# Kernel optimization log

Hardware: AMD Instinct MI355X
Metric: run time of the kernel (lower is better)

## Reference

```python
import jax, jax.numpy as jnp
import numpy as np

B, T, D, N = 4, 2048, 1024, 8
H = D // N


def _rope_tables(t, d, dtype=jnp.float32):
    inv_freq = 1.0 / (10000.0 ** (jnp.arange(0, d, 2, dtype=jnp.float32) / d))
    pos = jnp.arange(t, dtype=jnp.float32)
    ang = jnp.einsum('i,j->ij', pos, inv_freq)  # [T, D/2]
    cos = jnp.concatenate([jnp.cos(ang), jnp.cos(ang)], axis=-1).astype(dtype)  # [T, D]
    sin = jnp.concatenate([jnp.sin(ang), jnp.sin(ang)], axis=-1).astype(dtype)
    return cos, sin


def setup_inputs() -> dict:
    key = jax.random.key(0)
    kx, kq, kk, kv = jax.random.split(key, 4)
    s = 1.0 / np.sqrt(D)
    x = jax.random.normal(kx, (B, T, D), dtype=jnp.float32)
    wq = jax.random.normal(kq, (D, D), dtype=jnp.float32) * s
    wk = jax.random.normal(kk, (D, D), dtype=jnp.float32) * s
    wv = jax.random.normal(kv, (D, D), dtype=jnp.float32) * s
    cos, sin = _rope_tables(T, D)
    return {"x": x, "wq": wq, "wk": wk, "wv": wv, "cos": cos, "sin": sin}


def _rotate_half(z):
    # torch: view(..., -1, 2); x1=even idx, x2=odd idx; cat((-x2, x1), -1)
    return jnp.concatenate([-z[..., 1::2], z[..., 0::2]], axis=-1)


def reference(x, wq, wk, wv, cos, sin):
    b, t, c = x.shape
    n, h = N, H
    # nn.Linear(bias=False): y = x @ W.T
    q = jnp.einsum('btc,dc->btd', x, wq)
    k = jnp.einsum('btc,dc->btd', x, wk)
    v = jnp.einsum('btc,dc->btd', x, wv)
    q = q * cos + _rotate_half(q) * sin
    k = k * cos + _rotate_half(k) * sin
    q = q.reshape(b, t, n, h).transpose(0, 2, 1, 3)  # [b,n,t,h]
    k = k.reshape(b, t, n, h).transpose(0, 2, 1, 3)
    v = v.reshape(b, t, n, h).transpose(0, 2, 1, 3)
    scale = 1.0 / jnp.sqrt(jnp.asarray(h, dtype=q.dtype))
    scores = jnp.einsum('bnqh,bnkh->bnqk', q, k) * scale
    causal = jnp.tril(jnp.ones((t, t), dtype=bool))
    scores = jnp.where(causal, scores, jnp.finfo(scores.dtype).min)
    p = jax.nn.softmax(scores, axis=-1)
    out = jnp.einsum('bnqk,bnkh->bnqh', p, v)
    return out.transpose(0, 2, 1, 3).reshape(b, t, c)
```

## Files before the change

kernel.cpp:

```cpp
#include <hip/hip_runtime.h>

typedef unsigned short u16;
typedef unsigned int u32;
typedef _Float16 F16;
typedef __attribute__((ext_vector_type(8))) _Float16 h8v;
typedef __attribute__((ext_vector_type(4))) _Float16 h4v;
typedef __attribute__((ext_vector_type(4))) float f32x4;

#define DEV __device__ __forceinline__

DEV void gld16(const void* g, void* l) {
  __builtin_amdgcn_global_load_lds((const __attribute__((address_space(1))) void*)g,
                                   (__attribute__((address_space(3))) void*)l, 16, 0, 0);
}
DEV f32x4 mfma16(h8v a, h8v b, f32x4 c) {
  return __builtin_amdgcn_mfma_f32_16x16x32_f16(a, b, c, 0, 0, 0);
}

__global__ void __launch_bounds__(256) k_split_all(const float* __restrict__ x,
                                                   const float* __restrict__ wq,
                                                   const float* __restrict__ wk,
                                                   const float* __restrict__ wv,
                                                   F16* __restrict__ xh, F16* __restrict__ wh) {
  int i = blockIdx.x * 256 + threadIdx.x;
  const float* src; F16* dst; int li;
  if (i < 1048576)      { src = x;  dst = xh;            li = i; }
  else if (i < 1179648) { src = wq; dst = wh;            li = i - 1048576; }
  else if (i < 1310720) { src = wk; dst = wh + 1048576;  li = i - 1179648; }
  else                  { src = wv; dst = wh + 2097152;  li = i - 1310720; }
  const float4* p = (const float4*)src + (size_t)li * 2;
  float4 a = p[0], b = p[1];
  float v[8] = {a.x, a.y, a.z, a.w, b.x, b.y, b.z, b.w};
  h8v o;
#pragma unroll
  for (int j = 0; j < 8; ++j) o[j] = (F16)v[j];
  ((h8v*)dst)[li] = o;
}

__global__ void __launch_bounds__(256, 3) k_gemm_qkv(
    const F16* __restrict__ A, const F16* __restrict__ W,
    F16* __restrict__ qf, F16* __restrict__ kf, F16* __restrict__ vf) {
  __shared__ F16 lds[16384];
  F16* sA = lds;
  F16* sB = lds + 8192;
  const int tid = threadIdx.x;
  const int lane = tid & 63, w = tid >> 6;
  const int wm = w >> 1, wn = w & 1;
  const int l15 = lane & 15, g = lane >> 4;
  const int bid = blockIdx.x;
  const int mt = bid & 63, nt = bid >> 6;
  const F16* B = W + (size_t)(nt >> 3) * 1048576;
  F16* C = (nt < 8) ? qf : (nt < 16) ? kf : vf;
  const int m0 = mt * 128;
  const int n0 = (nt & 7) * 128;

  f32x4 acc[4][4] = {};

  for (int kt = 0; kt < 16; ++kt) {
    const int k0 = kt * 64;
#pragma unroll
    for (int p = 0; p < 4; ++p) {
      int u = p * 256 + tid;
      int row = u >> 3, jp = u & 7;
      int j = jp ^ (row & 7);
      size_t ga = (size_t)(m0 + row) * 1024 + k0 + j * 8;
      size_t gb = (size_t)(n0 + row) * 1024 + k0 + j * 8;
      gld16(A + ga, sA + u * 8);
      gld16(B + gb, sB + u * 8);
    }
    __syncthreads();
#pragma unroll
    for (int ks = 0; ks < 2; ++ks) {
      h8v fa[4], fb[4];
#pragma unroll
      for (int mf = 0; mf < 4; ++mf) {
        int row = wm * 64 + mf * 16 + l15;
        int off = row * 64 + (((ks * 4 + g) ^ (row & 7)) * 8);
        fa[mf] = *(const h8v*)(sA + off);
      }
#pragma unroll
      for (int nf = 0; nf < 4; ++nf) {
        int row = wn * 64 + nf * 16 + l15;
        int off = row * 64 + (((ks * 4 + g) ^ (row & 7)) * 8);
        fb[nf] = *(const h8v*)(sB + off);
      }
#pragma unroll
      for (int mf = 0; mf < 4; ++mf)
#pragma unroll
        for (int nf = 0; nf < 4; ++nf)
          acc[mf][nf] = mfma16(fa[mf], fb[nf], acc[mf][nf]);
    }
    __syncthreads();
  }
#pragma unroll
  for (int mf = 0; mf < 4; ++mf)
#pragma unroll
    for (int nf = 0; nf < 4; ++nf)
#pragma unroll
      for (int r = 0; r < 4; ++r) {
        int m = m0 + wm * 64 + mf * 16 + g * 4 + r;
        int n = n0 + wn * 64 + nf * 16 + l15;
        C[(size_t)m * 1024 + n] = (F16)acc[mf][nf][r];
      }
}

__global__ void __launch_bounds__(256) k_prep(const F16* __restrict__ qf, const F16* __restrict__ kf,
                                              const F16* __restrict__ vf,
                                              const float* __restrict__ cs, const float* __restrict__ sn,
                                              F16* __restrict__ qg, F16* __restrict__ kg,
                                              F16* __restrict__ vtg, float QS) {
  __shared__ float smem[8256];
  const int bid = blockIdx.x;
  const int tid = threadIdx.x;
  if (bid < 8192) {
    float* sq = smem;
    float* sk = smem + 1024;
    const int b = bid >> 11, t = bid & 2047;
    {
      h4v qi = ((const h4v*)(qf + (size_t)bid * 1024))[tid];
      h4v ki = ((const h4v*)(kf + (size_t)bid * 1024))[tid];
#pragma unroll
      for (int j = 0; j < 4; ++j) { sq[tid * 4 + j] = (float)qi[j]; sk[tid * 4 + j] = (float)ki[j]; }
    }
    __syncthreads();
    const int i0 = tid * 4;
    float4 c4 = ((const float4*)(cs + (size_t)t * 1024))[tid];
    float4 s4 = ((const float4*)(sn + (size_t)t * 1024))[tid];
    float cc[4] = {c4.x, c4.y, c4.z, c4.w};
    float ss[4] = {s4.x, s4.y, s4.z, s4.w};
    h4v qv, kv;
#pragma unroll
    for (int j = 0; j < 4; ++j) {
      int i = i0 + j;
      float zq, zk;
      if (i < 512) { zq = sq[i] * cc[j] - sq[2 * i + 1] * ss[j];
                     zk = sk[i] * cc[j] - sk[2 * i + 1] * ss[j]; }
      else         { zq = sq[i] * cc[j] + sq[2 * (i - 512)] * ss[j];
                     zk = sk[i] * cc[j] + sk[2 * (i - 512)] * ss[j]; }
      qv[j] = (F16)(zq * QS);
      kv[j] = (F16)zk;
    }
    const int n = i0 >> 7, hh = i0 & 127;
    const size_t o = ((size_t)(b * 8 + n) * 2048 + t) * 128 + hh;
    *(h4v*)(qg + o) = qv;
    *(h4v*)(kg + o) = kv;
  } else {
    const int vb = bid - 8192;
    const int tt = vb & 31, bn = vb >> 5;
    const int b = bn >> 3, n = bn & 7;
    const int t0 = tt * 64;
    float (*s)[129] = (float(*)[129])smem;
#pragma unroll
    for (int r8 = 0; r8 < 4; ++r8) {
      int row = r8 * 16 + (tid >> 4);
      int c8 = tid & 15;
      h8v v = *(const h8v*)(vf + ((size_t)b * 2048 + t0 + row) * 1024 + n * 128 + c8 * 8);
#pragma unroll
      for (int k = 0; k < 8; ++k) s[row][c8 * 8 + k] = (float)v[k];
    }
    __syncthreads();
    const int h = tid >> 1, half = tid & 1;
    const size_t ob = ((size_t)bn * 128 + h) * 2048 + t0 + half * 32;
    h8v o[4];
#pragma unroll
    for (int j = 0; j < 32; ++j) o[j >> 3][j & 7] = (F16)s[half * 32 + j][h];
#pragma unroll
    for (int jj = 0; jj < 4; ++jj) *(h8v*)(vtg + ob + jj * 8) = o[jj];
  }
}

__global__ void __launch_bounds__(256, 4) k_attn(const F16* __restrict__ Q, const F16* __restrict__ K,
                                                 const F16* __restrict__ Vt, float* __restrict__ Out) {
  const int bid = blockIdx.x;
  const int bn = bid & 31;
  const int o = bid >> 5;
  int qt;
  if (o < 8)       qt = 31 - o;
  else if (o < 16) qt = o - 8;
  else if (o < 24) qt = 39 - o;
  else             qt = o - 16;
  const int b = bn >> 3, n = bn & 7;
  const int q0 = qt * 64;
  const int tid = threadIdx.x;
  const int lane = tid & 63, w = tid >> 6;
  const int l15 = lane & 15, g = lane >> 4;

  __shared__ F16 sm[20480];
  F16* sK = sm;
  F16* sV = sm + 8192;
  F16* sP = sm + 16384 + w * 1024;

  h8v fq[4];
  {
    const size_t qoff = ((size_t)bn * 2048 + (q0 + w * 16 + l15)) * 128 + g * 8;
#pragma unroll
    for (int hs = 0; hs < 4; ++hs) fq[hs] = *(const h8v*)(Q + qoff + hs * 32);
  }

  const size_t kbase = (size_t)bn * 2048 * 128;
  const F16* kS[4]; const F16* vS[4]; F16* kD[4]; F16* vD[4];
#pragma unroll
  for (int p = 0; p < 4; ++p) {
    int u = p * 256 + tid;
    { int row = u >> 4, jp = u & 15, j = jp ^ (row & 15);
      kS[p] = K + kbase + (size_t)row * 128 + j * 8;
      kD[p] = sK + u * 8; }
    { int row = u >> 3, jp = u & 7, j = jp ^ (row & 7);
      vS[p] = Vt + kbase + (size_t)row * 2048 + j * 8;
      vD[p] = sV + u * 8; }
  }

  f32x4 ot[8] = {};
  float mrun = -1e30f;
  float lrun = 0.f;
  const int nkv = qt + 1;

  for (int kv = 0; kv < nkv; ++kv) {
    const int k0 = kv * 64;
#pragma unroll
    for (int p = 0; p < 4; ++p) {
      gld16(kS[p], kD[p]);
      gld16(vS[p], vD[p]);
      kS[p] += 8192;
      vS[p] += 64;
    }
    __syncthreads();

    f32x4 st[4] = {};
#pragma unroll
    for (int f = 0; f < 4; ++f) {
      const int row = f * 16 + l15;
      const F16* bk = sK + row * 128;
#pragma unroll
      for (int hs = 0; hs < 4; ++hs) {
        const int j = (((hs * 4 + g) ^ (row & 15)) * 8);
        st[f] = mfma16(*(const h8v*)(bk + j), fq[hs], st[f]);
      }
    }

    {
      const int qg = q0 + w * 16 + l15;
      if (k0 + 63 > q0 + w * 16) {
#pragma unroll
        for (int f = 0; f < 4; ++f)
#pragma unroll
          for (int r = 0; r < 4; ++r)
            if (k0 + f * 16 + g * 4 + r > qg) st[f][r] = -1e30f;
      }
      float tm = -1e30f;
#pragma unroll
      for (int f = 0; f < 4; ++f)
#pragma unroll
        for (int r = 0; r < 4; ++r) tm = fmaxf(tm, st[f][r]);
      tm = fmaxf(tm, __shfl_xor(tm, 16));
      tm = fmaxf(tm, __shfl_xor(tm, 32));
      float corr = 1.f;
      const bool resc = !__all(tm <= mrun + 8.0f);
      if (resc) {
        const float mn = fmaxf(mrun, tm);
        corr = exp2f(mrun - mn);
        mrun = mn;
      }
      float ps = 0.f;
      const int q = l15;
#pragma unroll
      for (int f = 0; f < 4; ++f) {
        h4v p4;
#pragma unroll
        for (int r = 0; r < 4; ++r) {
          float p = exp2f(st[f][r] - mrun);
          ps += p;
          p4[r] = (F16)p;
        }
        const int off = q * 64 + (((2 * f + (g >> 1)) ^ (q & 7)) * 8) + (g & 1) * 4;
        *(h4v*)(sP + off) = p4;
      }
      ps += __shfl_xor(ps, 16);
      ps += __shfl_xor(ps, 32);
      lrun = lrun * corr + ps;
      if (resc) {
#pragma unroll
        for (int hf = 0; hf < 8; ++hf) {
          ot[hf][0] *= corr; ot[hf][1] *= corr;
          ot[hf][2] *= corr; ot[hf][3] *= corr;
        }
      }
    }
    asm volatile("" ::: "memory");

    h8v fp[2];
    {
      const int q = l15;
#pragma unroll
      for (int c = 0; c < 2; ++c) {
        const int off = q * 64 + (((4 * c + g) ^ (q & 7)) * 8);
        fp[c] = *(const h8v*)(sP + off);
      }
    }
#pragma unroll
    for (int hf = 0; hf < 8; ++hf) {
      const int row = hf * 16 + l15;
      const int sw = row & 7;
#pragma unroll
      for (int c = 0; c < 2; ++c) {
        const int off = row * 64 + (((4 * c + g) ^ sw) * 8);
        ot[hf] = mfma16(*(const h8v*)(sV + off), fp[c], ot[hf]);
      }
    }
    __syncthreads();
  }

  {
    const float inv = 1.0f / lrun;
    const int qrow = q0 + w * 16 + l15;
    const size_t ob = ((size_t)b * 2048 + qrow) * 1024 + n * 128;
#pragma unroll
    for (int hf = 0; hf < 8; ++hf) {
      float4 o4;
      o4.x = ot[hf][0] * inv; o4.y = ot[hf][1] * inv;
      o4.z = ot[hf][2] * inv; o4.w = ot[hf][3] * inv;
      *(float4*)(Out + ob + hf * 16 + g * 4) = o4;
    }
  }
}

extern "C" void kernel_launch(void* const* d_in, const int* in_sizes, int n_in,
                              void* d_out, int out_size, void* d_ws, size_t ws_size,
                              hipStream_t stream) {
  const float* x  = (const float*)d_in[0];
  const float* wq = (const float*)d_in[1];
  const float* wk = (const float*)d_in[2];
  const float* wv = (const float*)d_in[3];
  const float* cs = (const float*)d_in[4];
  const float* sn = (const float*)d_in[5];
  float* out = (float*)d_out;

  F16* xh  = (F16*)d_ws;
  F16* wh  = xh + 8388608;
  F16* qf  = wh + 3145728;
  F16* kf  = qf + 8388608;
  F16* vf  = kf + 8388608;
  F16* kg  = vf + 8388608;
  F16* vtg = kg + 8388608;
  F16* qg  = xh;

  if (ws_size < (size_t)106954752) return;

  const float QS = 0.08838834764831845f * 1.4426950408889634f;

  k_split_all<<<5632, 256, 0, stream>>>(x, wq, wk, wv, xh, wh);
  k_gemm_qkv<<<1536, 256, 0, stream>>>(xh, wh, qf, kf, vf);
  k_prep<<<9216, 256, 0, stream>>>(qf, kf, vf, cs, sn, qg, kg, vtg, QS);
  k_attn<<<1024, 256, 0, stream>>>(qg, kg, vtg, out);
}
```

Before: 257.6 us.

## Split long causal attention tiles across KV segments with a merge kernel

```diff
diff --git a/kernel.cpp b/kernel.cpp
--- a/kernel.cpp
+++ b/kernel.cpp
@@ -16,6 +16,9 @@
 DEV f32x4 mfma16(h8v a, h8v b, f32x4 c) {
   return __builtin_amdgcn_mfma_f32_16x16x32_f16(a, b, c, 0, 0, 0);
 }
+
+__device__ __constant__ int QT_TAB[24]  = {15,7,14,14,13,6,12,11, 15,13,12,10,10,9,11,5, 0,1,2,3,8,9,8,4};
+__device__ __constant__ int SEG_TAB[24] = { 0,2, 0, 1, 1,2, 1, 1,  1, 0, 0, 0, 1,0, 0,2, 2,2,2,2,1,1,0,2};
 
 __global__ void __launch_bounds__(256) k_split_all(const float* __restrict__ x,
                                                    const float* __restrict__ wq,
@@ -169,23 +172,23 @@
   }
 }
 
-__global__ void __launch_bounds__(256, 4) k_attn(const F16* __restrict__ Q, const F16* __restrict__ K,
-                                                 const F16* __restrict__ Vt, float* __restrict__ Out) {
+__global__ void __launch_bounds__(512, 6) k_attn(const F16* __restrict__ Q, const F16* __restrict__ K,
+                                                 const F16* __restrict__ Vt, float* __restrict__ Out,
+                                                 float* __restrict__ Pot, float2* __restrict__ Pml) {
   const int bid = blockIdx.x;
   const int bn = bid & 31;
-  const int o = bid >> 5;
-  int qt;
-  if (o < 8)       qt = 31 - o;
-  else if (o < 16) qt = o - 8;
-  else if (o < 24) qt = 39 - o;
-  else             qt = o - 16;
+  const int ord = bid >> 5;
+  const int qt = QT_TAB[ord];
+  const int seg = SEG_TAB[ord];
   const int b = bn >> 3, n = bn & 7;
-  const int q0 = qt * 64;
+  const int q0 = qt * 128;
+  const int kv0 = (seg == 1) ? qt + 1 : 0;
+  const int kv1 = (seg == 0) ? qt + 1 : 2 * qt + 2;
   const int tid = threadIdx.x;
   const int lane = tid & 63, w = tid >> 6;
   const int l15 = lane & 15, g = lane >> 4;
 
-  __shared__ F16 sm[20480];
+  __shared__ F16 sm[24576];
   F16* sK = sm;
   F16* sV = sm + 8192;
   F16* sP = sm + 16384 + w * 1024;
@@ -198,27 +201,26 @@
   }
 
   const size_t kbase = (size_t)bn * 2048 * 128;
-  const F16* kS[4]; const F16* vS[4]; F16* kD[4]; F16* vD[4];
-#pragma unroll
-  for (int p = 0; p < 4; ++p) {
-    int u = p * 256 + tid;
+  const F16* kS[2]; const F16* vS[2]; F16* kD[2]; F16* vD[2];
+#pragma unroll
+  for (int p = 0; p < 2; ++p) {
+    int u = p * 512 + tid;
     { int row = u >> 4, jp = u & 15, j = jp ^ (row & 15);
-      kS[p] = K + kbase + (size_t)row * 128 + j * 8;
+      kS[p] = K + kbase + (size_t)(kv0 * 64 + row) * 128 + j * 8;
       kD[p] = sK + u * 8; }
     { int row = u >> 3, jp = u & 7, j = jp ^ (row & 7);
-      vS[p] = Vt + kbase + (size_t)row * 2048 + j * 8;
+      vS[p] = Vt + kbase + (size_t)row * 2048 + kv0 * 64 + j * 8;
       vD[p] = sV + u * 8; }
   }
 
   f32x4 ot[8] = {};
   float mrun = -1e30f;
   float lrun = 0.f;
-  const int nkv = qt + 1;
-
-  for (int kv = 0; kv < nkv; ++kv) {
+
+  for (int kv = kv0; kv < kv1; ++kv) {
     const int k0 = kv * 64;
 #pragma unroll
-    for (int p = 0; p < 4; ++p) {
+    for (int p = 0; p < 2; ++p) {
       gld16(kS[p], kD[p]);
       gld16(vS[p], vD[p]);
       kS[p] += 8192;
@@ -310,10 +312,10 @@
     __syncthreads();
   }
 
-  {
+  const int ql = w * 16 + l15;
+  if (seg == 2) {
     const float inv = 1.0f / lrun;
-    const int qrow = q0 + w * 16 + l15;
-    const size_t ob = ((size_t)b * 2048 + qrow) * 1024 + n * 128;
+    const size_t ob = ((size_t)b * 2048 + q0 + ql) * 1024 + n * 128;
 #pragma unroll
     for (int hf = 0; hf < 8; ++hf) {
       float4 o4;
@@ -321,6 +323,43 @@
       o4.z = ot[hf][2] * inv; o4.w = ot[hf][3] * inv;
       *(float4*)(Out + ob + hf * 16 + g * 4) = o4;
     }
+  } else {
+    const int pq = bn * 8 + (qt - 8);
+    float* pr = Pot + ((size_t)(pq * 2 + seg) * 128 + ql) * 128;
+#pragma unroll
+    for (int hf = 0; hf < 8; ++hf) {
+      float4 o4;
+      o4.x = ot[hf][0]; o4.y = ot[hf][1]; o4.z = ot[hf][2]; o4.w = ot[hf][3];
+      *(float4*)(pr + hf * 16 + g * 4) = o4;
+    }
+    if (g == 0) Pml[(pq * 2 + seg) * 128 + ql] = make_float2(mrun, lrun);
+  }
+}
+
+__global__ void __launch_bounds__(256) k_merge(const float* __restrict__ Pot,
+                                               const float2* __restrict__ Pml,
+                                               float* __restrict__ Out) {
+  const int pq = blockIdx.x;
+  const int bn = pq >> 3, qt = (pq & 7) + 8;
+  const int b = bn >> 3, n = bn & 7;
+  const int t = threadIdx.x;
+  const int q = t >> 1, hb = (t & 1) * 64;
+  const float2 ml0 = Pml[(pq * 2 + 0) * 128 + q];
+  const float2 ml1 = Pml[(pq * 2 + 1) * 128 + q];
+  const float M = fmaxf(ml0.x, ml1.x);
+  const float s0 = exp2f(ml0.x - M), s1 = exp2f(ml1.x - M);
+  const float inv = 1.0f / (ml0.y * s0 + ml1.y * s1);
+  const float4* p0 = (const float4*)(Pot + ((size_t)(pq * 2 + 0) * 128 + q) * 128 + hb);
+  const float4* p1 = (const float4*)(Pot + ((size_t)(pq * 2 + 1) * 128 + q) * 128 + hb);
+  float4* op = (float4*)(Out + ((size_t)b * 2048 + qt * 128 + q) * 1024 + n * 128 + hb);
+#pragma unroll
+  for (int j = 0; j < 16; ++j) {
+    float4 a = p0[j], c = p1[j], o4;
+    o4.x = (a.x * s0 + c.x * s1) * inv;
+    o4.y = (a.y * s0 + c.y * s1) * inv;
+    o4.z = (a.z * s0 + c.z * s1) * inv;
+    o4.w = (a.w * s0 + c.w * s1) * inv;
+    op[j] = o4;
   }
 }
 
@@ -343,13 +382,16 @@
   F16* kg  = vf + 8388608;
   F16* vtg = kg + 8388608;
   F16* qg  = xh;
-
-  if (ws_size < (size_t)106954752) return;
+  float*  pot = (float*)(vtg + 8388608);
+  float2* pml = (float2*)(pot + 8388608);
+
+  if (ws_size < (size_t)141033472) return;
 
   const float QS = 0.08838834764831845f * 1.4426950408889634f;
 
   k_split_all<<<5632, 256, 0, stream>>>(x, wq, wk, wv, xh, wh);
   k_gemm_qkv<<<1536, 256, 0, stream>>>(xh, wh, qf, kf, vf);
   k_prep<<<9216, 256, 0, stream>>>(qf, kf, vf, cs, sn, qg, kg, vtg, QS);
-  k_attn<<<1024, 256, 0, stream>>>(qg, kg, vtg, out);
-}
+  k_attn<<<768, 512, 0, stream>>>(qg, kg, vtg, out, pot, pml);
+  k_merge<<<256, 256, 0, stream>>>(pot, pml, out);
+}
```

Measured after the change: 354.0 us. 37.4% more time.
